# Kernel tuning notes

Measured on AMD Instinct MI355X. Metric: run time of the kernel, lower is better.

## Reference

```python
import jax, jax.numpy as jnp
from jax import lax
import numpy as np

B, T, F = 32, 8192, 16
HID = 128
OUT = 24
K1 = 10


def setup_inputs() -> dict:
    key = jax.random.key(0)
    ks = jax.random.split(key, 5)
    x = jax.random.normal(ks[0], (B, T, F), dtype=jnp.float32)
    # Conv1d(F -> HID, kernel=10): weight (O, I, K), bias (O,)
    w1 = jax.random.normal(ks[1], (HID, F, K1), dtype=jnp.float32) * (1.0 / np.sqrt(F * K1))
    b1 = jax.random.normal(ks[2], (HID,), dtype=jnp.float32) * 0.01
    # Linear(HID*10 -> OUT): weight (OUT, HID*10), bias (OUT,)
    wf = jax.random.normal(ks[3], (OUT, HID * K1), dtype=jnp.float32) * (1.0 / np.sqrt(HID * K1))
    bf = jax.random.normal(ks[4], (OUT,), dtype=jnp.float32) * 0.01
    return {"x": x, "w1": w1, "b1": b1, "wf": wf, "bf": bf}


def reference(x, w1, b1, wf, bf):
    # x: (B, T, F) -> (B, F, T)
    xc = jnp.transpose(x, (0, 2, 1))
    # Conv1d k=10, pad=9 -> length T+9
    h = lax.conv_general_dilated(
        xc, w1, window_strides=(1,), padding=[(9, 9)],
        dimension_numbers=("NCH", "OIH", "NCH")) + b1[None, :, None]  # (B, HID, T+9)
    # out[:, :x.shape[2], :] keeps the first T timesteps
    h = h[:, :, :x.shape[1]]
    h = jnp.concatenate([jnp.repeat(h[:, :, :1], 9, axis=2), h], axis=2)
    # Per-step Linear over flattened 10-step windows == valid conv with k=10.
    # flatten order of window (10, C) is time-major: col index = t*C + c
    kf = jnp.transpose(wf.reshape(wf.shape[0], K1, -1), (0, 2, 1))  # (OUT, HID, 10)
    y = lax.conv_general_dilated(
        h, kf, window_strides=(1,), padding="VALID",
        dimension_numbers=("NCH", "OIH", "NCH")) + bf[None, :, None]  # (B, OUT, T)
    return jnp.transpose(y, (0, 2, 1))  # (B, T, OUT)
```

## Files before the change

kernel.cpp:

```cpp
#include <hip/hip_runtime.h>

#define B_   32
#define T_   8192
#define F_   16
#define OUT_ 24
#define K1_  10
#define ND   19
#define JP   32
#define PADL 24
#define XROWS_TOT (PADL + T_ + 8)

#define WS_BC_OFF   20480
#define WS_E_OFF    20576
#define WS_W1T_OFF  144992
#define WS_XBF_OFF  226944

typedef short short8 __attribute__((ext_vector_type(8)));
typedef float float4v __attribute__((ext_vector_type(4)));

__device__ __forceinline__ unsigned short f2bf(float f) {
    unsigned u = __builtin_bit_cast(unsigned, f);
    unsigned r = (u + 0x7fffu + ((u >> 16) & 1u)) >> 16;
    return (unsigned short)r;
}

__device__ __forceinline__ short8 cvt8(float4 f0, float4 f1) {
    short8 v;
    v[0] = (short)f2bf(f0.x); v[1] = (short)f2bf(f0.y);
    v[2] = (short)f2bf(f0.z); v[3] = (short)f2bf(f0.w);
    v[4] = (short)f2bf(f1.x); v[5] = (short)f2bf(f1.y);
    v[6] = (short)f2bf(f1.z); v[7] = (short)f2bf(f1.w);
    return v;
}

__global__ __launch_bounds__(256) void pre_kernel(const float* __restrict__ x,
                                                  const float* __restrict__ w1,
                                                  unsigned short* __restrict__ xbf,
                                                  float* __restrict__ w1t,
                                                  unsigned short* __restrict__ w2pk) {
    int bx = blockIdx.x;
    int tid = threadIdx.x;
    if (bx < 1028) {
        int id = bx * 256 + tid;
        if (id >= B_ * XROWS_TOT) return;
        int b = id / XROWS_TOT, r = id - b * XROWS_TOT;
        unsigned short* dst = xbf + (size_t)id * 16;
        int t = r - PADL;
        short8 v0 = short8{0,0,0,0,0,0,0,0}, v1 = v0;
        if (t >= 0 && t < T_) {
            const float4* p = (const float4*)(x + ((long)b * T_ + t) * 16);
            float4 f0 = p[0], f1 = p[1], f2 = p[2], f3 = p[3];
            v0 = cvt8(f0, f1);
            v1 = cvt8(f2, f3);
        }
        *(short8*)dst = v0;
        *(short8*)(dst + 8) = v1;
    } else if (bx < 1108) {
        int idx = (bx - 1028) * 256 + tid;
        float v = w1[idx];
        int c = idx / 160;
        int rem = idx - c * 160;
        int i = rem / 10;
        int k = rem - i * 10;
        w1t[(k * 16 + i) * 128 + c] = v;
    } else {
        int idx = (bx - 1108) * 256 + tid;
        ((unsigned*)w2pk)[idx] = 0;
    }
}

__global__ __launch_bounds__(256) void prep_kernel(const float* __restrict__ w1t,
                                                   const float* __restrict__ b1,
                                                   const float* __restrict__ wf,
                                                   const float* __restrict__ bf,
                                                   unsigned short* __restrict__ w2pk,
                                                   float* __restrict__ bcg,
                                                   float* __restrict__ Eg) {
    int tid = threadIdx.x;
    int lane = tid & 63;
    int wid = blockIdx.x * 4 + (tid >> 6);

    if (wid < 456) {
        int j = wid / ND, d = wid % ND;
        float p[16];
#pragma unroll
        for (int i = 0; i < 16; ++i) p[i] = 0.f;
        int klo = d - 9 > 0 ? d - 9 : 0;
        int khi = d < 9 ? d : 9;
        for (int k = klo; k <= khi; ++k) {
            float w0 = wf[j * 1280 + k * 128 + lane];
            float w1v = wf[j * 1280 + k * 128 + 64 + lane];
            const float* wb = w1t + (d - k) * 16 * 128;
#pragma unroll
            for (int i = 0; i < 16; ++i)
                p[i] = fmaf(w0, wb[i * 128 + lane], fmaf(w1v, wb[i * 128 + 64 + lane], p[i]));
        }
#pragma unroll
        for (int i = 0; i < 16; ++i) {
            p[i] += __shfl_xor(p[i], 1);
            p[i] += __shfl_xor(p[i], 2);
            p[i] += __shfl_xor(p[i], 4);
            p[i] += __shfl_xor(p[i], 8);
            p[i] += __shfl_xor(p[i], 16);
            p[i] += __shfl_xor(p[i], 32);
        }
        if (lane < 16) {
            float v = p[0];
#pragma unroll
            for (int i = 1; i < 16; ++i)
                if (lane == i) v = p[i];
            int kk = d * 16 + lane;
            int ks = kk >> 5, r = kk & 31;
            int quad = r >> 3, z = r & 7;
            int tbl = j >> 4, jj = j & 15;
            int lt = jj + quad * 16;
            w2pk[((tbl * 10 + ks) * 64 + lt) * 8 + z] = f2bf(v);
        }
    } else if (wid < 480) {
        int j = wid - 456;
        float s0 = 0.f, s1 = 0.f;
#pragma unroll
        for (int k = 0; k < K1_; ++k) {
            s0 += wf[j * 1280 + k * 128 + lane];
            s1 += wf[j * 1280 + k * 128 + 64 + lane];
        }
        float s = s0 * b1[lane] + s1 * b1[64 + lane];
        s += __shfl_xor(s, 1);
        s += __shfl_xor(s, 2);
        s += __shfl_xor(s, 4);
        s += __shfl_xor(s, 8);
        s += __shfl_xor(s, 16);
        s += __shfl_xor(s, 32);
        if (lane == 0) bcg[j] = bf[j] + s;
    } else {
        int eidx = wid - 480;
        int t = eidx / 216;
        int rem = eidx % 216;
        int j = rem / 9, tau = rem % 9;
        float p[16];
#pragma unroll
        for (int i = 0; i < 16; ++i) p[i] = 0.f;
        for (int k = 0; k < K1_; ++k) {
            int u = t + k - 9; if (u < 0) u = 0;
            if (tau > u) continue;
            int kap = tau + 9 - u;
            float w0 = wf[j * 1280 + k * 128 + lane];
            float w1v = wf[j * 1280 + k * 128 + 64 + lane];
            const float* wb = w1t + kap * 16 * 128;
#pragma unroll
            for (int i = 0; i < 16; ++i)
                p[i] = fmaf(w0, wb[i * 128 + lane], fmaf(w1v, wb[i * 128 + 64 + lane], p[i]));
        }
#pragma unroll
        for (int i = 0; i < 16; ++i) {
            p[i] += __shfl_xor(p[i], 1);
            p[i] += __shfl_xor(p[i], 2);
            p[i] += __shfl_xor(p[i], 4);
            p[i] += __shfl_xor(p[i], 8);
            p[i] += __shfl_xor(p[i], 16);
            p[i] += __shfl_xor(p[i], 32);
        }
        if (lane < 16) {
            float v = p[0];
#pragma unroll
            for (int i = 1; i < 16; ++i)
                if (lane == i) v = p[i];
            Eg[((t * OUT_ + j) * 9 + tau) * 16 + lane] = v;
        }
    }
}

__global__ __launch_bounds__(256) void main_kernel(const unsigned short* __restrict__ xbf,
                                                   const unsigned short* __restrict__ w2pk,
                                                   const float* __restrict__ bcg,
                                                   float* __restrict__ out,
                                                   const float* __restrict__ x,
                                                   const float* __restrict__ Eg) {
    int tid = threadIdx.x;
    int b = blockIdx.y;

    if (blockIdx.x == 32) {
        if (tid >= 9 * OUT_) return;
        int t = tid / OUT_, j = tid % OUT_;
        const float4* xv = (const float4*)(x + (long)b * T_ * F_);
        const float4* ev = (const float4*)(Eg + (long)tid * 144);
        float ax = 0.f, ay = 0.f, az = 0.f, aw = 0.f;
#pragma unroll
        for (int q = 0; q < 36; ++q) {
            float4 e = ev[q];
            float4 v = xv[q];
            ax = fmaf(e.x, v.x, ax);
            ay = fmaf(e.y, v.y, ay);
            az = fmaf(e.z, v.z, az);
            aw = fmaf(e.w, v.w, aw);
        }
        out[((long)b * T_ + t) * OUT_ + j] = bcg[j] + ((ax + ay) + (az + aw));
        return;
    }

    int lane = tid & 63, w = tid >> 6;
    int t0 = blockIdx.x * 256;

    int m = lane & 15, quad = lane >> 4;
    int ih = (quad & 1) * 8;
    int dq = quad >> 1;
    const unsigned short* xb = xbf + (size_t)b * XROWS_TOT * 16;
    int base = PADL + t0 + w * 64 + m + dq - 18;
    const unsigned short* pk0 = w2pk + lane * 8;
    const unsigned short* pk1 = w2pk + 5120 + lane * 8;

    short8 B0[10], B1[10];
#pragma unroll
    for (int ks = 0; ks < 10; ++ks) {
        B0[ks] = *(const short8*)(pk0 + ks * 512);
        B1[ks] = *(const short8*)(pk1 + ks * 512);
    }

    float4v acc[4][2];
#pragma unroll
    for (int mt = 0; mt < 4; ++mt)
#pragma unroll
        for (int nt = 0; nt < 2; ++nt) acc[mt][nt] = float4v{0.f, 0.f, 0.f, 0.f};

#pragma unroll
    for (int ks = 0; ks < 10; ++ks) {
#pragma unroll
        for (int mt = 0; mt < 4; ++mt) {
            short8 a = *(const short8*)(xb + (size_t)(base + mt * 16 + 2 * ks) * 16 + ih);
            acc[mt][0] = __builtin_amdgcn_mfma_f32_16x16x32_bf16(a, B0[ks], acc[mt][0], 0, 0, 0);
            acc[mt][1] = __builtin_amdgcn_mfma_f32_16x16x32_bf16(a, B1[ks], acc[mt][1], 0, 0, 0);
        }
    }

    long outb = (long)b * T_;
    float bc0 = bcg[m];
    float bc1 = (m < 8) ? bcg[16 + m] : 0.f;
    bool edge = (blockIdx.x == 0);
#pragma unroll
    for (int mt = 0; mt < 4; ++mt) {
        int trow = t0 + w * 64 + mt * 16 + quad * 4;
#pragma unroll
        for (int reg = 0; reg < 4; ++reg) {
            int t = trow + reg;
            if (!edge || t >= 9) {
                float* o = out + (outb + t) * OUT_;
                o[m] = acc[mt][0][reg] + bc0;
                if (m < 8) o[16 + m] = acc[mt][1][reg] + bc1;
            }
        }
    }
}

extern "C" void kernel_launch(void* const* d_in, const int* in_sizes, int n_in,
                              void* d_out, int out_size, void* d_ws, size_t ws_size,
                              hipStream_t stream) {
    const float* x  = (const float*)d_in[0];
    const float* w1 = (const float*)d_in[1];
    const float* b1 = (const float*)d_in[2];
    const float* wf = (const float*)d_in[3];
    const float* bf = (const float*)d_in[4];
    float* out = (float*)d_out;
    unsigned short* w2pk = (unsigned short*)d_ws;
    float* bcg = (float*)((char*)d_ws + WS_BC_OFF);
    float* Eg  = (float*)((char*)d_ws + WS_E_OFF);
    float* w1t = (float*)((char*)d_ws + WS_W1T_OFF);
    unsigned short* xbf = (unsigned short*)((char*)d_ws + WS_XBF_OFF);

    hipLaunchKernelGGL(pre_kernel, dim3(1148), dim3(256), 0, stream,
                       x, w1, xbf, w1t, w2pk);
    hipLaunchKernelGGL(prep_kernel, dim3(606), dim3(256), 0, stream,
                       w1t, b1, wf, bf, w2pk, bcg, Eg);
    hipLaunchKernelGGL(main_kernel, dim3(33, B_), dim3(256), 0, stream,
                       xbf, w2pk, bcg, out, x, Eg);
}
```

Baseline: 102.7 us.

## Stage bf16 input window in LDS, split halves, swap MFMA operands for vector stores

The bf16 copy of x is split into two planar arrays holding the low and high 8 features. The main kernel now stages a 536-row window per 512-timestep block in shared memory, instead of each lane re-reading overlapping global rows for every kernel tap. The MFMA operands are swapped so each lane holds four consecutive output channels, which allows float4 output stores. Each block now covers 512 timesteps with 8 M-tiles per wave, halving the grid and doubling accumulators. This adds a __syncthreads and LDS traffic, and launch_bounds(256,2) may pressure registers.

```diff
diff --git a/kernel.cpp b/kernel.cpp
--- a/kernel.cpp
+++ b/kernel.cpp
@@ -9,11 +9,14 @@
 #define JP   32
 #define PADL 24
 #define XROWS_TOT (PADL + T_ + 8)
+#define TB   512
+#define WROWS 536
 
 #define WS_BC_OFF   20480
 #define WS_E_OFF    20576
 #define WS_W1T_OFF  144992
-#define WS_XBF_OFF  226944
+#define WS_XLO_OFF  226944
+#define WS_XHI_OFF  (WS_XLO_OFF + B_ * XROWS_TOT * 8 * 2)
 
 typedef short short8 __attribute__((ext_vector_type(8)));
 typedef float float4v __attribute__((ext_vector_type(4)));
@@ -35,7 +38,8 @@
 
 __global__ __launch_bounds__(256) void pre_kernel(const float* __restrict__ x,
                                                   const float* __restrict__ w1,
-                                                  unsigned short* __restrict__ xbf,
+                                                  unsigned short* __restrict__ xlo,
+                                                  unsigned short* __restrict__ xhi,
                                                   float* __restrict__ w1t,
                                                   unsigned short* __restrict__ w2pk) {
     int bx = blockIdx.x;
@@ -44,7 +48,6 @@
         int id = bx * 256 + tid;
         if (id >= B_ * XROWS_TOT) return;
         int b = id / XROWS_TOT, r = id - b * XROWS_TOT;
-        unsigned short* dst = xbf + (size_t)id * 16;
         int t = r - PADL;
         short8 v0 = short8{0,0,0,0,0,0,0,0}, v1 = v0;
         if (t >= 0 && t < T_) {
@@ -53,8 +56,8 @@
             v0 = cvt8(f0, f1);
             v1 = cvt8(f2, f3);
         }
-        *(short8*)dst = v0;
-        *(short8*)(dst + 8) = v1;
+        *(short8*)(xlo + (size_t)id * 8) = v0;
+        *(short8*)(xhi + (size_t)id * 8) = v1;
     } else if (bx < 1108) {
         int idx = (bx - 1028) * 256 + tid;
         float v = w1[idx];
@@ -170,16 +173,17 @@
     }
 }
 
-__global__ __launch_bounds__(256) void main_kernel(const unsigned short* __restrict__ xbf,
-                                                   const unsigned short* __restrict__ w2pk,
-                                                   const float* __restrict__ bcg,
-                                                   float* __restrict__ out,
-                                                   const float* __restrict__ x,
-                                                   const float* __restrict__ Eg) {
+__global__ __launch_bounds__(256, 2) void main_kernel(const unsigned short* __restrict__ xlo,
+                                                      const unsigned short* __restrict__ xhi,
+                                                      const unsigned short* __restrict__ w2pk,
+                                                      const float* __restrict__ bcg,
+                                                      float* __restrict__ out,
+                                                      const float* __restrict__ x,
+                                                      const float* __restrict__ Eg) {
     int tid = threadIdx.x;
     int b = blockIdx.y;
 
-    if (blockIdx.x == 32) {
+    if (blockIdx.x == 16) {
         if (tid >= 9 * OUT_) return;
         int t = tid / OUT_, j = tid % OUT_;
         const float4* xv = (const float4*)(x + (long)b * T_ * F_);
@@ -198,54 +202,68 @@
         return;
     }
 
+    __shared__ short xls[2 * WROWS * 8];
+    int t0 = blockIdx.x * TB;
+    int gbase = PADL + t0 - 18;
+
+    for (int idx = tid; idx < 2 * WROWS; idx += 256) {
+        int h = idx >= WROWS;
+        int row = h ? idx - WROWS : idx;
+        const unsigned short* src = (h ? xhi : xlo) + ((size_t)b * XROWS_TOT + gbase + row) * 8;
+        short8 v = *(const short8*)src;
+        *(short8*)(xls + (h * WROWS + row) * 8) = v;
+    }
+
     int lane = tid & 63, w = tid >> 6;
-    int t0 = blockIdx.x * 256;
-
-    int m = lane & 15, quad = lane >> 4;
-    int ih = (quad & 1) * 8;
-    int dq = quad >> 1;
-    const unsigned short* xb = xbf + (size_t)b * XROWS_TOT * 16;
-    int base = PADL + t0 + w * 64 + m + dq - 18;
+    int t = lane & 15, q = lane >> 4;
+    int h = q & 1, qh = q >> 1;
+
     const unsigned short* pk0 = w2pk + lane * 8;
     const unsigned short* pk1 = w2pk + 5120 + lane * 8;
-
-    short8 B0[10], B1[10];
+    short8 W0[10], W1[10];
 #pragma unroll
     for (int ks = 0; ks < 10; ++ks) {
-        B0[ks] = *(const short8*)(pk0 + ks * 512);
-        B1[ks] = *(const short8*)(pk1 + ks * 512);
-    }
-
-    float4v acc[4][2];
-#pragma unroll
-    for (int mt = 0; mt < 4; ++mt)
-#pragma unroll
-        for (int nt = 0; nt < 2; ++nt) acc[mt][nt] = float4v{0.f, 0.f, 0.f, 0.f};
+        W0[ks] = *(const short8*)(pk0 + ks * 512);
+        W1[ks] = *(const short8*)(pk1 + ks * 512);
+    }
+
+    __syncthreads();
+
+    const short* ap = xls + (h * WROWS + w * 128 + t + qh) * 8;
+
+    float4v acc[8][2];
+#pragma unroll
+    for (int mt = 0; mt < 8; ++mt) {
+        acc[mt][0] = float4v{0.f, 0.f, 0.f, 0.f};
+        acc[mt][1] = float4v{0.f, 0.f, 0.f, 0.f};
+    }
 
 #pragma unroll
     for (int ks = 0; ks < 10; ++ks) {
 #pragma unroll
-        for (int mt = 0; mt < 4; ++mt) {
-            short8 a = *(const short8*)(xb + (size_t)(base + mt * 16 + 2 * ks) * 16 + ih);
-            acc[mt][0] = __builtin_amdgcn_mfma_f32_16x16x32_bf16(a, B0[ks], acc[mt][0], 0, 0, 0);
-            acc[mt][1] = __builtin_amdgcn_mfma_f32_16x16x32_bf16(a, B1[ks], acc[mt][1], 0, 0, 0);
+        for (int mt = 0; mt < 8; ++mt) {
+            short8 xf = *(const short8*)(ap + (mt * 16 + 2 * ks) * 8);
+            acc[mt][0] = __builtin_amdgcn_mfma_f32_16x16x32_bf16(W0[ks], xf, acc[mt][0], 0, 0, 0);
+            acc[mt][1] = __builtin_amdgcn_mfma_f32_16x16x32_bf16(W1[ks], xf, acc[mt][1], 0, 0, 0);
         }
     }
 
     long outb = (long)b * T_;
-    float bc0 = bcg[m];
-    float bc1 = (m < 8) ? bcg[16 + m] : 0.f;
+    float4 bc0 = *(const float4*)(bcg + q * 4);
+    float4 bc1 = (q < 2) ? *(const float4*)(bcg + 16 + q * 4) : make_float4(0.f, 0.f, 0.f, 0.f);
     bool edge = (blockIdx.x == 0);
 #pragma unroll
-    for (int mt = 0; mt < 4; ++mt) {
-        int trow = t0 + w * 64 + mt * 16 + quad * 4;
-#pragma unroll
-        for (int reg = 0; reg < 4; ++reg) {
-            int t = trow + reg;
-            if (!edge || t >= 9) {
-                float* o = out + (outb + t) * OUT_;
-                o[m] = acc[mt][0][reg] + bc0;
-                if (m < 8) o[16 + m] = acc[mt][1][reg] + bc1;
+    for (int mt = 0; mt < 8; ++mt) {
+        int t_out = t0 + w * 128 + mt * 16 + t;
+        if (!edge || t_out >= 9) {
+            float* o = out + (outb + t_out) * OUT_;
+            float4 v0 = make_float4(acc[mt][0][0] + bc0.x, acc[mt][0][1] + bc0.y,
+                                    acc[mt][0][2] + bc0.z, acc[mt][0][3] + bc0.w);
+            *(float4*)(o + q * 4) = v0;
+            if (q < 2) {
+                float4 v1 = make_float4(acc[mt][1][0] + bc1.x, acc[mt][1][1] + bc1.y,
+                                        acc[mt][1][2] + bc1.z, acc[mt][1][3] + bc1.w);
+                *(float4*)(o + 16 + q * 4) = v1;
             }
         }
     }
@@ -264,12 +282,13 @@
     float* bcg = (float*)((char*)d_ws + WS_BC_OFF);
     float* Eg  = (float*)((char*)d_ws + WS_E_OFF);
     float* w1t = (float*)((char*)d_ws + WS_W1T_OFF);
-    unsigned short* xbf = (unsigned short*)((char*)d_ws + WS_XBF_OFF);
+    unsigned short* xlo = (unsigned short*)((char*)d_ws + WS_XLO_OFF);
+    unsigned short* xhi = (unsigned short*)((char*)d_ws + WS_XHI_OFF);
 
     hipLaunchKernelGGL(pre_kernel, dim3(1148), dim3(256), 0, stream,
-                       x, w1, xbf, w1t, w2pk);
+                       x, w1, xlo, xhi, w1t, w2pk);
     hipLaunchKernelGGL(prep_kernel, dim3(606), dim3(256), 0, stream,
                        w1t, b1, wf, bf, w2pk, bcg, Eg);
-    hipLaunchKernelGGL(main_kernel, dim3(33, B_), dim3(256), 0, stream,
-                       xbf, w2pk, bcg, out, x, Eg);
-}
+    hipLaunchKernelGGL(main_kernel, dim3(17, B_), dim3(256), 0, stream,
+                       xlo, xhi, w2pk, bcg, out, x, Eg);
+}
```

New measurement: 99.32 us. -3.3%, faster.
